# Kernel optimization log

Measured on AMD Instinct MI355X. Metric: run time of the kernel, lower is better.

The kernel has to match this reference:

```python
import jax, jax.numpy as jnp
import numpy as np

B, S, D, H, E, K = 4, 1024, 1024, 4096, 8, 2


def setup_inputs() -> dict:
    key = jax.random.key(0)
    ks = jax.random.split(key, 5)
    std = 0.02
    return {
        "x": jax.random.normal(ks[0], (B, S, D), dtype=jnp.float32),
        "router_W": jax.random.normal(ks[1], (D, E), dtype=jnp.float32) * std,
        "W_in": jax.random.normal(ks[2], (E, D, H), dtype=jnp.float32) * std,
        "b_in": jnp.zeros((E, H), dtype=jnp.float32),
        "W_out": jax.random.normal(ks[3], (E, H, D), dtype=jnp.float32) * std,
        "b_out": jnp.zeros((E, D), dtype=jnp.float32),
    }


def reference(x, router_W, W_in, b_in, W_out, b_out):
    # ---- routing ----
    logits = jnp.einsum("bsd,de->bse", x, router_W)          # [B,S,E]
    probs = jax.nn.softmax(logits, axis=-1)                    # [B,S,E]
    top_p, top_i = jax.lax.top_k(probs, K)                     # [B,S,K]
    top_p = top_p / (jnp.sum(top_p, axis=-1, keepdims=True) + 1e-8)
    one_hot = jax.nn.one_hot(top_i, E, dtype=x.dtype)          # [B,S,K,E]
    combine = jnp.sum(one_hot * top_p[..., None], axis=-2)     # [B,S,E] per-expert weight

    # ---- experts (original runs full batch through every selected expert;
    #      with E=8, K=2 all experts are active, so run all densely) ----
    h = jnp.einsum("bsd,edh->ebsh", x, W_in) + b_in[:, None, None, :]
    h = jax.nn.gelu(h, approximate=False)
    y = jnp.einsum("ebsh,ehd->ebsd", h, W_out) + b_out[:, None, None, :]
    out = jnp.einsum("bse,ebsd->bsd", combine, y)              # weighted combine

    # ---- load-balancing aux loss ----
    expert_usage = jnp.mean(one_hot, axis=(0, 1, 2))           # f_i, fraction of routed slots
    avg_probs = jnp.mean(probs, axis=(0, 1))                   # P_i
    aux_loss = E * jnp.sum(avg_probs * expert_usage)
    return out, aux_loss
```

## Files before the change

kernel.cpp:

```cpp
#include <hip/hip_runtime.h>
#include <hip/hip_bf16.h>
#include <math.h>

#define B_ 4
#define S_ 1024
#define T_ (B_ * S_)
#define D_ 1024
#define H_ 4096
#define E_ 8
#define K_ 2
#define A_ (T_ * K_)
#define MAXT_ 72

typedef __bf16 bf16x8_t __attribute__((ext_vector_type(8)));
typedef float f32x4_t __attribute__((ext_vector_type(4)));

__device__ inline unsigned short f2bf(float f) {
    __hip_bfloat16 h = __float2bfloat16(f);
    return *reinterpret_cast<unsigned short*>(&h);
}

__device__ __forceinline__ void gl2lds16(const unsigned short* g, unsigned short* l) {
    auto* gp = reinterpret_cast<const __attribute__((address_space(1))) unsigned int*>(
        reinterpret_cast<uintptr_t>(g));
    auto* lp = reinterpret_cast<__attribute__((address_space(3))) unsigned int*>(
        reinterpret_cast<uintptr_t>(l));
    __builtin_amdgcn_global_load_lds(gp, lp, 16, 0, 0);
}


__global__ void router_kernel(const float* __restrict__ x, const float* __restrict__ rw,
                              int* __restrict__ tok_e, float* __restrict__ tok_w,
                              int* __restrict__ counts_pad, float* __restrict__ probs_pad) {
    __shared__ float s_probs[E_];
    __shared__ int s_counts[E_];
    const int tid = threadIdx.x;
    if (tid < E_) { s_probs[tid] = 0.f; s_counts[tid] = 0; }
    __syncthreads();
    const int wave = tid >> 6;
    const int lane = tid & 63;

    float wprob[E_];
    int wcount[E_];
#pragma unroll
    for (int e = 0; e < E_; ++e) { wprob[e] = 0.f; wcount[e] = 0; }

    for (int tt = 0; tt < 4; ++tt) {
        const int token = blockIdx.x * 16 + wave * 4 + tt;
        const float* xr = x + (long)token * D_;
        float acc[E_];
#pragma unroll
        for (int e = 0; e < E_; ++e) acc[e] = 0.f;
        for (int i = 0; i < D_ / 64; ++i) {
            int d = i * 64 + lane;
            float xv = xr[d];
            const float* w = rw + (long)d * E_;
#pragma unroll
            for (int e = 0; e < E_; ++e) acc[e] += xv * w[e];
        }
#pragma unroll
        for (int e = 0; e < E_; ++e) {
            for (int off = 32; off > 0; off >>= 1)
                acc[e] += __shfl_down(acc[e], off);
        }
        if (lane == 0) {
            float m = acc[0];
            for (int e = 1; e < E_; ++e) m = fmaxf(m, acc[e]);
            float p[E_], s = 0.f;
            for (int e = 0; e < E_; ++e) { p[e] = expf(acc[e] - m); s += p[e]; }
            float inv = 1.f / s;
            for (int e = 0; e < E_; ++e) { p[e] *= inv; wprob[e] += p[e]; }
            int i0 = 0;
            for (int e = 1; e < E_; ++e) if (p[e] > p[i0]) i0 = e;
            int i1 = (i0 == 0) ? 1 : 0;
            for (int e = 0; e < E_; ++e) if (e != i0 && p[e] > p[i1]) i1 = e;
            float w0 = p[i0], w1 = p[i1];
            float inv2 = 1.f / (w0 + w1 + 1e-8f);
            tok_e[token * 2] = i0;
            tok_e[token * 2 + 1] = i1;
            tok_w[token * 2] = w0 * inv2;
            tok_w[token * 2 + 1] = w1 * inv2;
            wcount[i0]++; wcount[i1]++;
        }
    }
    if (lane == 0) {
#pragma unroll
        for (int e = 0; e < E_; ++e) {
            atomicAdd(&s_probs[e], wprob[e]);
            if (wcount[e]) atomicAdd(&s_counts[e], wcount[e]);
        }
    }
    __syncthreads();
    if (tid < E_) {
        atomicAdd(&probs_pad[tid * 32], s_probs[tid]);
        if (s_counts[tid]) atomicAdd(&counts_pad[tid * 32], s_counts[tid]);
    }
}

__global__ void offsets_aux_kernel(const int* __restrict__ counts_pad,
                                   const float* __restrict__ probs_pad,
                                   int* __restrict__ offsets,
                                   int* __restrict__ tile_e, int* __restrict__ tile_m,
                                   int* __restrict__ n_tiles, float* __restrict__ aux_out) {
    if (threadIdx.x == 0 && blockIdx.x == 0) {
        int run = 0, t = 0;
        for (int e = 0; e < E_; ++e) {
            int c = counts_pad[e * 32];
            offsets[e] = run;
            for (int m0 = 0; m0 < c; m0 += 128) {
                tile_e[t] = e; tile_m[t] = m0; ++t;
            }
            run += c;
        }
        offsets[E_] = run;
        *n_tiles = t;
        float aux = 0.f;
        for (int e = 0; e < E_; ++e)
            aux += (probs_pad[e * 32] / (float)T_) * ((float)counts_pad[e * 32] / (float)A_);
        *aux_out = (float)E_ * aux;
    }
}

__global__ void scatter_kernel(const int* __restrict__ tok_e, const float* __restrict__ tok_w,
                               const int* __restrict__ offsets, int* __restrict__ cursors_pad,
                               int* __restrict__ perm_token, float* __restrict__ perm_weight,
                               int* __restrict__ inv_pos) {
    int i = blockIdx.x * blockDim.x + threadIdx.x;
    int lane = threadIdx.x & 63;
    int e = tok_e[i];
    float w = tok_w[i];
    unsigned long long bal[E_];
#pragma unroll
    for (int q = 0; q < E_; ++q) bal[q] = __ballot(e == q);
    unsigned long long below = (1ull << lane) - 1ull;
    int rank = __popcll(bal[e] & below);
    int base = 0;
    if (lane < E_) {
        int c = __popcll(bal[lane]);
        if (c) base = atomicAdd(&cursors_pad[lane * 32], c);
    }
    int mybase = __shfl(base, e);
    int pos = offsets[e] + mybase + rank;
    perm_token[pos] = i >> 1;
    perm_weight[pos] = w;
    inv_pos[i] = pos;
}

__global__ void cast_x_kernel(const float* __restrict__ x, unsigned short* __restrict__ xb) {
    long i = (long)blockIdx.x * blockDim.x + threadIdx.x;
    float4 v = reinterpret_cast<const float4*>(x)[i];
    unsigned long long packed = (unsigned long long)f2bf(v.x)
        | ((unsigned long long)f2bf(v.y) << 16)
        | ((unsigned long long)f2bf(v.z) << 32)
        | ((unsigned long long)f2bf(v.w) << 48);
    reinterpret_cast<unsigned long long*>(xb)[i] = packed;
}

__global__ void transpose_cast_kernel(const float* __restrict__ in, unsigned short* __restrict__ out,
                                      int R, int C) {
    __shared__ float tile[32][33];
    long e = blockIdx.z;
    const float* in_e = in + e * (long)R * C;
    unsigned short* out_e = out + e * (long)R * C;
    int x0 = blockIdx.x * 32;
    int y0 = blockIdx.y * 32;
    int tx = threadIdx.x, ty = threadIdx.y;
#pragma unroll
    for (int i = 0; i < 4; ++i)
        tile[ty + i * 8][tx] = in_e[(long)(y0 + ty + i * 8) * C + x0 + tx];
    __syncthreads();
#pragma unroll
    for (int i = 0; i < 4; ++i)
        out_e[(long)(x0 + ty + i * 8) * R + y0 + tx] = f2bf(tile[tx][ty + i * 8]);
}

template <int PHASE>
__launch_bounds__(256, 4)
__global__ void moe_gemm_kernel(const unsigned short* __restrict__ A_src,
                                const unsigned short* __restrict__ B_src,
                                const float* __restrict__ bias,
                                const int* __restrict__ offsets,
                                const int* __restrict__ tile_e, const int* __restrict__ tile_m,
                                const int* __restrict__ p_ntiles,
                                const int* __restrict__ perm_token,
                                const float* __restrict__ perm_weight,
                                unsigned short* __restrict__ h_buf,
                                float* __restrict__ y_perm) {
    constexpr int Ksz = (PHASE == 1) ? D_ : H_;
    constexpr int Nsz = (PHASE == 1) ? H_ : D_;
    constexpr int NTX = (Nsz / 128) / 8;
    const int id = blockIdx.x;
    const int c = id & 7;
    const int r = id >> 3;
    const int mt = r % MAXT_;
    if (mt >= *p_ntiles) return;
    const int nt = c * NTX + r / MAXT_;
    const int e = tile_e[mt];
    const int m0 = tile_m[mt];
    const int off_e = offsets[e];
    const int n_e = offsets[e + 1] - off_e;
    const int n0 = nt * 128;

    __shared__ __attribute__((aligned(16))) unsigned short lds_a[2 * 128 * 32];
    __shared__ __attribute__((aligned(16))) unsigned short lds_b[2 * 128 * 32];

    const int tid = threadIdx.x;
    const int lane = tid & 63;
    const int wave = tid >> 6;
    const int wm = (wave >> 1) * 64;
    const int wn = (wave & 1) * 64;
    const int lrow = lane & 15;
    const int kg = lane >> 4;

    const unsigned short* gA[2];
    const unsigned short* gB[2];
    unsigned short* ldsA[2];
    unsigned short* ldsB[2];
#pragma unroll
    for (int j = 0; j < 2; ++j) {
        const int g = j * 4 + wave;
        const int rr = g * 16 + (lane >> 2);
        const int ch = lane & 3;
        const int sc = ch ^ ((rr >> 1) & 3);
        int m_loc = m0 + rr;
        int m_cl = (m_loc < n_e) ? m_loc : (n_e - 1);
        int pos = off_e + m_cl;
        long arow;
        if (PHASE == 1) arow = (long)perm_token[pos] * Ksz;
        else            arow = (long)pos * Ksz;
        gA[j] = A_src + arow + sc * 8;
        gB[j] = B_src + (long)e * Nsz * Ksz + (long)(n0 + rr) * Ksz + sc * 8;
        ldsA[j] = lds_a + g * 512;
        ldsB[j] = lds_b + g * 512;
    }

    int a_off[4], b_off[4];
#pragma unroll
    for (int i = 0; i < 4; ++i) {
        const int rr = wm + i * 16 + lrow;
        a_off[i] = rr * 32 + ((kg ^ ((rr >> 1) & 3)) * 8);
        const int cc = wn + i * 16 + lrow;
        b_off[i] = cc * 32 + ((kg ^ ((cc >> 1) & 3)) * 8);
    }

    f32x4_t acc[4][4];
#pragma unroll
    for (int i = 0; i < 4; ++i)
#pragma unroll
        for (int j = 0; j < 4; ++j)
            acc[i][j] = (f32x4_t){0.f, 0.f, 0.f, 0.f};

    gl2lds16(gA[0], ldsA[0]);
    gl2lds16(gA[1], ldsA[1]);
    gl2lds16(gB[0], ldsB[0]);
    gl2lds16(gB[1], ldsB[1]);

    for (int k0 = 0; k0 < Ksz; k0 += 32) {
        const int cur = (k0 >> 5) & 1;
        __syncthreads();
        if (k0 + 32 < Ksz) {
            const int nxt = cur ^ 1;
            gl2lds16(gA[0] + k0 + 32, ldsA[0] + nxt * 4096);
            gl2lds16(gA[1] + k0 + 32, ldsA[1] + nxt * 4096);
            gl2lds16(gB[0] + k0 + 32, ldsB[0] + nxt * 4096);
            gl2lds16(gB[1] + k0 + 32, ldsB[1] + nxt * 4096);
        }
        const unsigned short* la = lds_a + cur * 4096;
        const unsigned short* lb = lds_b + cur * 4096;
        bf16x8_t a_frag[4], b_frag[4];
#pragma unroll
        for (int i = 0; i < 4; ++i) {
            a_frag[i] = *reinterpret_cast<const bf16x8_t*>(&la[a_off[i]]);
            b_frag[i] = *reinterpret_cast<const bf16x8_t*>(&lb[b_off[i]]);
        }
#pragma unroll
        for (int i = 0; i < 4; ++i)
#pragma unroll
            for (int j = 0; j < 4; ++j)
                acc[i][j] = __builtin_amdgcn_mfma_f32_16x16x32_bf16(a_frag[i], b_frag[j], acc[i][j], 0, 0, 0);
    }

    const float* bias_e = bias + (long)e * Nsz;
#pragma unroll
    for (int i = 0; i < 4; ++i) {
#pragma unroll
        for (int rq = 0; rq < 4; ++rq) {
            int row_loc = wm + i * 16 + kg * 4 + rq;
            int m_loc = m0 + row_loc;
            if (m_loc >= n_e) continue;
            int pos = off_e + m_loc;
            if (PHASE == 1) {
#pragma unroll
                for (int j = 0; j < 4; ++j) {
                    int n = n0 + wn + j * 16 + lrow;
                    float v = acc[i][j][rq] + bias_e[n];
                    v = 0.5f * v * (1.0f + erff(v * 0.70710678118654752440f));
                    h_buf[(long)pos * Nsz + n] = f2bf(v);
                }
            } else {
                float wgt = perm_weight[pos];
#pragma unroll
                for (int j = 0; j < 4; ++j) {
                    int n = n0 + wn + j * 16 + lrow;
                    y_perm[(long)pos * Nsz + n] = (acc[i][j][rq] + bias_e[n]) * wgt;
                }
            }
        }
    }
}

__global__ void combine_kernel(const float* __restrict__ y_perm, const int* __restrict__ inv_pos,
                               float* __restrict__ out) {
    int t = blockIdx.x;
    int d4 = threadIdx.x;
    int p0 = inv_pos[t * 2];
    int p1 = inv_pos[t * 2 + 1];
    float4 a = reinterpret_cast<const float4*>(y_perm + (long)p0 * D_)[d4];
    float4 b = reinterpret_cast<const float4*>(y_perm + (long)p1 * D_)[d4];
    float4 o = {a.x + b.x, a.y + b.y, a.z + b.z, a.w + b.w};
    reinterpret_cast<float4*>(out + (long)t * D_)[d4] = o;
}

extern "C" void kernel_launch(void* const* d_in, const int* in_sizes, int n_in,
                              void* d_out, int out_size, void* d_ws, size_t ws_size,
                              hipStream_t stream) {
    const float* x        = (const float*)d_in[0];
    const float* router_W = (const float*)d_in[1];
    const float* W_in     = (const float*)d_in[2];
    const float* b_in     = (const float*)d_in[3];
    const float* W_out    = (const float*)d_in[4];
    const float* b_out    = (const float*)d_in[5];
    float* out = (float*)d_out;

    char* ws = (char*)d_ws;
    size_t off = 0;
    auto alloc = [&](size_t bytes) -> void* {
        void* p = ws + off;
        off += (bytes + 255) & ~(size_t)255;
        return p;
    };

    char* ctrl = (char*)alloc(4096);
    int* counts_pad   = (int*)ctrl;
    float* probs_pad  = (float*)(ctrl + 1024);
    int* cursors_pad  = (int*)(ctrl + 2048);
    int* offsets      = (int*)(ctrl + 3072);
    int* tile_e       = (int*)(ctrl + 3200);
    int* tile_m       = (int*)(ctrl + 3584);
    int* n_tiles      = (int*)(ctrl + 3968);
    int* tok_e         = (int*)alloc((size_t)A_ * 4);
    float* tok_w       = (float*)alloc((size_t)A_ * 4);
    int* perm_token    = (int*)alloc((size_t)A_ * 4);
    float* perm_weight = (float*)alloc((size_t)A_ * 4);
    int* inv_pos       = (int*)alloc((size_t)A_ * 4);
    unsigned short* x_bf    = (unsigned short*)alloc((size_t)T_ * D_ * 2);
    unsigned short* w_in_t  = (unsigned short*)alloc((size_t)E_ * D_ * H_ * 2);
    unsigned short* w_out_t = (unsigned short*)alloc((size_t)E_ * D_ * H_ * 2);
    unsigned short* h_buf   = (unsigned short*)alloc((size_t)A_ * H_ * 2);
    float* y_perm           = (float*)alloc((size_t)A_ * D_ * 4);

    hipMemsetAsync(ctrl, 0, 4096, stream);

    cast_x_kernel<<<(T_ * D_ / 4) / 256, 256, 0, stream>>>(x, x_bf);
    transpose_cast_kernel<<<dim3(H_ / 32, D_ / 32, E_), dim3(32, 8), 0, stream>>>(W_in, w_in_t, D_, H_);
    transpose_cast_kernel<<<dim3(D_ / 32, H_ / 32, E_), dim3(32, 8), 0, stream>>>(W_out, w_out_t, H_, D_);
    router_kernel<<<T_ / 16, 256, 0, stream>>>(x, router_W, tok_e, tok_w, counts_pad, probs_pad);
    offsets_aux_kernel<<<1, 64, 0, stream>>>(counts_pad, probs_pad, offsets,
                                             tile_e, tile_m, n_tiles, out + (out_size - 1));
    scatter_kernel<<<A_ / 256, 256, 0, stream>>>(tok_e, tok_w, offsets, cursors_pad,
                                                 perm_token, perm_weight, inv_pos);

    moe_gemm_kernel<1><<<8 * MAXT_ * (H_ / 128 / 8), 256, 0, stream>>>(
        x_bf, w_in_t, b_in, offsets, tile_e, tile_m, n_tiles,
        perm_token, perm_weight, h_buf, y_perm);
    moe_gemm_kernel<2><<<8 * MAXT_ * (D_ / 128 / 8), 256, 0, stream>>>(
        h_buf, w_out_t, b_out, offsets, tile_e, tile_m, n_tiles,
        perm_token, perm_weight, h_buf, y_perm);
    combine_kernel<<<T_, 256, 0, stream>>>(y_perm, inv_pos, out);
}
```

Measured before the change: 661.1 us.

## Enlarge MoE GEMM tiles, triple-buffer K pipeline, add split-K and XCD remap

The grouped GEMM now uses 256x128 tiles with 512 threads, a K step of 64, and a three-stage global_load_lds pipeline with explicit barriers, setprio and waitcnt. Blocks are remapped so consecutive work lands on the same XCD. The second GEMM can split K in two into separate partial buffers when the workspace is large enough, and the combine kernel sums those partials. The weight transpose-cast kernel is rewritten with 64x64 tiles and vectorized loads and stores. The aim is better data reuse and MFMA utilisation, at the cost of more LDS, lower occupancy, padding waste on partial 256-row tiles, and extra partial-sum traffic when split-K is on.

Result: slower. 682.7 us (+3.3%).

```diff
diff --git a/kernel.cpp b/kernel.cpp
--- a/kernel.cpp
+++ b/kernel.cpp
@@ -10,10 +10,11 @@
 #define E_ 8
 #define K_ 2
 #define A_ (T_ * K_)
-#define MAXT_ 72
+#define NTM_ 40
 
 typedef __bf16 bf16x8_t __attribute__((ext_vector_type(8)));
 typedef float f32x4_t __attribute__((ext_vector_type(4)));
+typedef unsigned short u16x8_t __attribute__((ext_vector_type(8)));
 
 __device__ inline unsigned short f2bf(float f) {
     __hip_bfloat16 h = __float2bfloat16(f);
@@ -107,7 +108,7 @@
         for (int e = 0; e < E_; ++e) {
             int c = counts_pad[e * 32];
             offsets[e] = run;
-            for (int m0 = 0; m0 < c; m0 += 128) {
+            for (int m0 = 0; m0 < c; m0 += 256) {
                 tile_e[t] = e; tile_m[t] = m0; ++t;
             }
             run += c;
@@ -158,24 +159,36 @@
 
 __global__ void transpose_cast_kernel(const float* __restrict__ in, unsigned short* __restrict__ out,
                                       int R, int C) {
-    __shared__ float tile[32][33];
-    long e = blockIdx.z;
+    __shared__ float tile[64][65];
+    const long e = blockIdx.z;
     const float* in_e = in + e * (long)R * C;
     unsigned short* out_e = out + e * (long)R * C;
-    int x0 = blockIdx.x * 32;
-    int y0 = blockIdx.y * 32;
-    int tx = threadIdx.x, ty = threadIdx.y;
-#pragma unroll
-    for (int i = 0; i < 4; ++i)
-        tile[ty + i * 8][tx] = in_e[(long)(y0 + ty + i * 8) * C + x0 + tx];
+    const int c0 = blockIdx.x * 64;
+    const int r0 = blockIdx.y * 64;
+    const int tid = threadIdx.x;
+    const int c4 = (tid & 15) * 4;
+    const int rb = tid >> 4;
+#pragma unroll
+    for (int i = 0; i < 4; ++i) {
+        const int r = rb + i * 16;
+        const float4 v = *reinterpret_cast<const float4*>(&in_e[(long)(r0 + r) * C + c0 + c4]);
+        tile[r][c4] = v.x; tile[r][c4 + 1] = v.y; tile[r][c4 + 2] = v.z; tile[r][c4 + 3] = v.w;
+    }
     __syncthreads();
-#pragma unroll
-    for (int i = 0; i < 4; ++i)
-        out_e[(long)(x0 + ty + i * 8) * R + y0 + tx] = f2bf(tile[tx][ty + i * 8]);
-}
-
-template <int PHASE>
-__launch_bounds__(256, 4)
+    const int rs = (tid & 7) * 8;
+    const int cb = tid >> 3;
+#pragma unroll
+    for (int i = 0; i < 2; ++i) {
+        const int c = cb + i * 32;
+        u16x8_t p;
+#pragma unroll
+        for (int j = 0; j < 8; ++j) p[j] = f2bf(tile[rs + j][c]);
+        *reinterpret_cast<u16x8_t*>(&out_e[(long)(c0 + c) * R + r0 + rs]) = p;
+    }
+}
+
+template <int PHASE, int NSPLIT>
+__launch_bounds__(512, 2)
 __global__ void moe_gemm_kernel(const unsigned short* __restrict__ A_src,
                                 const unsigned short* __restrict__ B_src,
                                 const float* __restrict__ bias,
@@ -186,123 +199,186 @@
                                 const float* __restrict__ perm_weight,
                                 unsigned short* __restrict__ h_buf,
                                 float* __restrict__ y_perm) {
-    constexpr int Ksz = (PHASE == 1) ? D_ : H_;
-    constexpr int Nsz = (PHASE == 1) ? H_ : D_;
-    constexpr int NTX = (Nsz / 128) / 8;
+    constexpr int Ksz  = (PHASE == 1) ? D_ : H_;
+    constexpr int Kloc = (PHASE == 1) ? D_ : (H_ / NSPLIT);
+    constexpr int Nsz  = (PHASE == 1) ? H_ : D_;
+    constexpr int NT   = Kloc / 64;
+    constexpr int NTN  = Nsz / 128;
+
+    const int nwg = gridDim.x;
     const int id = blockIdx.x;
-    const int c = id & 7;
-    const int r = id >> 3;
-    const int mt = r % MAXT_;
+    const int q = nwg >> 3, r8 = nwg & 7;
+    const int xcd = id & 7, sub = id >> 3;
+    const int wg = (xcd < r8 ? xcd * (q + 1) : r8 * (q + 1) + (xcd - r8) * q) + sub;
+    const int mt = wg % NTM_;
     if (mt >= *p_ntiles) return;
-    const int nt = c * NTX + r / MAXT_;
+    const int rest = wg / NTM_;
+    const int nt = rest % NTN;
+    const int kh = rest / NTN;
     const int e = tile_e[mt];
     const int m0 = tile_m[mt];
     const int off_e = offsets[e];
     const int n_e = offsets[e + 1] - off_e;
     const int n0 = nt * 128;
-
-    __shared__ __attribute__((aligned(16))) unsigned short lds_a[2 * 128 * 32];
-    __shared__ __attribute__((aligned(16))) unsigned short lds_b[2 * 128 * 32];
+    const long k_base = (long)kh * Kloc;
+
+    __shared__ __attribute__((aligned(16))) unsigned short lds_a[3 * 256 * 64];
+    __shared__ __attribute__((aligned(16))) unsigned short lds_b[3 * 128 * 64];
 
     const int tid = threadIdx.x;
     const int lane = tid & 63;
     const int wave = tid >> 6;
-    const int wm = (wave >> 1) * 64;
-    const int wn = (wave & 1) * 64;
+    const int wr = wave >> 1;
+    const int wc = wave & 1;
     const int lrow = lane & 15;
     const int kg = lane >> 4;
 
-    const unsigned short* gA[2];
+    const unsigned short* gA[4];
     const unsigned short* gB[2];
-    unsigned short* ldsA[2];
-    unsigned short* ldsB[2];
-#pragma unroll
-    for (int j = 0; j < 2; ++j) {
-        const int g = j * 4 + wave;
-        const int rr = g * 16 + (lane >> 2);
-        const int ch = lane & 3;
-        const int sc = ch ^ ((rr >> 1) & 3);
-        int m_loc = m0 + rr;
-        int m_cl = (m_loc < n_e) ? m_loc : (n_e - 1);
-        int pos = off_e + m_cl;
+    int dstA[4], dstB[2];
+#pragma unroll
+    for (int j = 0; j < 4; ++j) {
+        const int chunk = j * 512 + tid;
+        const int rr = chunk >> 3;
+        const int ch = tid & 7;
+        const int m_loc = m0 + rr;
+        const int m_cl = (m_loc < n_e) ? m_loc : (n_e - 1);
+        const int pos = off_e + m_cl;
         long arow;
         if (PHASE == 1) arow = (long)perm_token[pos] * Ksz;
         else            arow = (long)pos * Ksz;
-        gA[j] = A_src + arow + sc * 8;
-        gB[j] = B_src + (long)e * Nsz * Ksz + (long)(n0 + rr) * Ksz + sc * 8;
-        ldsA[j] = lds_a + g * 512;
-        ldsB[j] = lds_b + g * 512;
-    }
-
-    int a_off[4], b_off[4];
-#pragma unroll
-    for (int i = 0; i < 4; ++i) {
-        const int rr = wm + i * 16 + lrow;
-        a_off[i] = rr * 32 + ((kg ^ ((rr >> 1) & 3)) * 8);
-        const int cc = wn + i * 16 + lrow;
-        b_off[i] = cc * 32 + ((kg ^ ((cc >> 1) & 3)) * 8);
-    }
+        gA[j] = A_src + arow + k_base + ((ch ^ (rr & 7)) * 8);
+        dstA[j] = (j * 512 + wave * 64) * 8;
+    }
+#pragma unroll
+    for (int j = 0; j < 2; ++j) {
+        const int chunk = j * 512 + tid;
+        const int rr = chunk >> 3;
+        const int ch = tid & 7;
+        gB[j] = B_src + (long)e * Nsz * Ksz + (long)(n0 + rr) * Ksz + k_base + ((ch ^ (rr & 7)) * 8);
+        dstB[j] = (j * 512 + wave * 64) * 8;
+    }
+
+    int aoff[2][4], boff[2][4];
+#pragma unroll
+    for (int kf = 0; kf < 2; ++kf)
+#pragma unroll
+        for (int i = 0; i < 4; ++i) {
+            const int r = wr * 64 + i * 16 + lrow;
+            aoff[kf][i] = r * 64 + (((kf * 4 + kg) ^ (r & 7)) * 8);
+            const int c = wc * 64 + i * 16 + lrow;
+            boff[kf][i] = c * 64 + (((kf * 4 + kg) ^ (c & 7)) * 8);
+        }
 
     f32x4_t acc[4][4];
 #pragma unroll
     for (int i = 0; i < 4; ++i)
 #pragma unroll
-        for (int j = 0; j < 4; ++j)
-            acc[i][j] = (f32x4_t){0.f, 0.f, 0.f, 0.f};
-
-    gl2lds16(gA[0], ldsA[0]);
-    gl2lds16(gA[1], ldsA[1]);
-    gl2lds16(gB[0], ldsB[0]);
-    gl2lds16(gB[1], ldsB[1]);
-
-    for (int k0 = 0; k0 < Ksz; k0 += 32) {
-        const int cur = (k0 >> 5) & 1;
-        __syncthreads();
-        if (k0 + 32 < Ksz) {
-            const int nxt = cur ^ 1;
-            gl2lds16(gA[0] + k0 + 32, ldsA[0] + nxt * 4096);
-            gl2lds16(gA[1] + k0 + 32, ldsA[1] + nxt * 4096);
-            gl2lds16(gB[0] + k0 + 32, ldsB[0] + nxt * 4096);
-            gl2lds16(gB[1] + k0 + 32, ldsB[1] + nxt * 4096);
-        }
-        const unsigned short* la = lds_a + cur * 4096;
-        const unsigned short* lb = lds_b + cur * 4096;
-        bf16x8_t a_frag[4], b_frag[4];
+        for (int j = 0; j < 4; ++j) acc[i][j] = (f32x4_t){0.f, 0.f, 0.f, 0.f};
+
+#pragma unroll
+    for (int tt = 0; tt < 2; ++tt) {
+        gl2lds16(gA[0] + tt * 64, lds_a + tt * 16384 + dstA[0]);
+        gl2lds16(gA[1] + tt * 64, lds_a + tt * 16384 + dstA[1]);
+        gl2lds16(gB[0] + tt * 64, lds_b + tt * 8192 + dstB[0]);
+        gl2lds16(gA[2] + tt * 64, lds_a + tt * 16384 + dstA[2]);
+        gl2lds16(gA[3] + tt * 64, lds_a + tt * 16384 + dstA[3]);
+        gl2lds16(gB[1] + tt * 64, lds_b + tt * 8192 + dstB[1]);
+    }
+    asm volatile("s_waitcnt vmcnt(6)" ::: "memory");
+    __builtin_amdgcn_s_barrier();
+
+    for (int t = 0; t < NT; ++t) {
+        const int s = t % 3;
+        const int s2 = (t + 2) % 3;
+        const unsigned short* la = lds_a + s * 16384;
+        const unsigned short* lb = lds_b + s * 8192;
+        const bool pf = (t + 2 < NT);
+
+        bf16x8_t a0[4], b0[4];
+#pragma unroll
+        for (int i = 0; i < 4; ++i) a0[i] = *reinterpret_cast<const bf16x8_t*>(la + aoff[0][i]);
+#pragma unroll
+        for (int i = 0; i < 4; ++i) b0[i] = *reinterpret_cast<const bf16x8_t*>(lb + boff[0][i]);
+        if (pf) {
+            gl2lds16(gA[0] + (t + 2) * 64, lds_a + s2 * 16384 + dstA[0]);
+            gl2lds16(gA[1] + (t + 2) * 64, lds_a + s2 * 16384 + dstA[1]);
+            gl2lds16(gB[0] + (t + 2) * 64, lds_b + s2 * 8192 + dstB[0]);
+        }
+        __builtin_amdgcn_s_barrier();
+        asm volatile("s_waitcnt lgkmcnt(0)" ::: "memory");
+        __builtin_amdgcn_sched_barrier(0);
+        __builtin_amdgcn_s_setprio(1);
+#pragma unroll
+        for (int i = 0; i < 4; ++i)
+#pragma unroll
+            for (int j = 0; j < 4; ++j)
+                acc[i][j] = __builtin_amdgcn_mfma_f32_16x16x32_bf16(a0[i], b0[j], acc[i][j], 0, 0, 0);
+        __builtin_amdgcn_s_setprio(0);
+        __builtin_amdgcn_s_barrier();
+
+        bf16x8_t a1[4], b1[4];
+#pragma unroll
+        for (int i = 0; i < 4; ++i) a1[i] = *reinterpret_cast<const bf16x8_t*>(la + aoff[1][i]);
+#pragma unroll
+        for (int i = 0; i < 4; ++i) b1[i] = *reinterpret_cast<const bf16x8_t*>(lb + boff[1][i]);
+        if (pf) {
+            gl2lds16(gA[2] + (t + 2) * 64, lds_a + s2 * 16384 + dstA[2]);
+            gl2lds16(gA[3] + (t + 2) * 64, lds_a + s2 * 16384 + dstA[3]);
+            gl2lds16(gB[1] + (t + 2) * 64, lds_b + s2 * 8192 + dstB[1]);
+        }
+        __builtin_amdgcn_s_barrier();
+        asm volatile("s_waitcnt lgkmcnt(0)" ::: "memory");
+        __builtin_amdgcn_sched_barrier(0);
+        __builtin_amdgcn_s_setprio(1);
+#pragma unroll
+        for (int i = 0; i < 4; ++i)
+#pragma unroll
+            for (int j = 0; j < 4; ++j)
+                acc[i][j] = __builtin_amdgcn_mfma_f32_16x16x32_bf16(a1[i], b1[j], acc[i][j], 0, 0, 0);
+        __builtin_amdgcn_s_setprio(0);
+        if (t + 1 < NT) {
+            if (t + 2 < NT) asm volatile("s_waitcnt vmcnt(6)" ::: "memory");
+            else            asm volatile("s_waitcnt vmcnt(0)" ::: "memory");
+        }
+        __builtin_amdgcn_s_barrier();
+    }
+
+    const float* bias_e = bias + (long)e * Nsz;
+    if (PHASE == 1) {
 #pragma unroll
         for (int i = 0; i < 4; ++i) {
-            a_frag[i] = *reinterpret_cast<const bf16x8_t*>(&la[a_off[i]]);
-            b_frag[i] = *reinterpret_cast<const bf16x8_t*>(&lb[b_off[i]]);
-        }
-#pragma unroll
-        for (int i = 0; i < 4; ++i)
-#pragma unroll
-            for (int j = 0; j < 4; ++j)
-                acc[i][j] = __builtin_amdgcn_mfma_f32_16x16x32_bf16(a_frag[i], b_frag[j], acc[i][j], 0, 0, 0);
-    }
-
-    const float* bias_e = bias + (long)e * Nsz;
-#pragma unroll
-    for (int i = 0; i < 4; ++i) {
-#pragma unroll
-        for (int rq = 0; rq < 4; ++rq) {
-            int row_loc = wm + i * 16 + kg * 4 + rq;
-            int m_loc = m0 + row_loc;
-            if (m_loc >= n_e) continue;
-            int pos = off_e + m_loc;
-            if (PHASE == 1) {
+#pragma unroll
+            for (int rq = 0; rq < 4; ++rq) {
+                const int row_loc = wr * 64 + i * 16 + kg * 4 + rq;
+                const int m_loc = m0 + row_loc;
+                if (m_loc >= n_e) continue;
+                const int pos = off_e + m_loc;
 #pragma unroll
                 for (int j = 0; j < 4; ++j) {
-                    int n = n0 + wn + j * 16 + lrow;
+                    const int n = n0 + wc * 64 + j * 16 + lrow;
                     float v = acc[i][j][rq] + bias_e[n];
                     v = 0.5f * v * (1.0f + erff(v * 0.70710678118654752440f));
                     h_buf[(long)pos * Nsz + n] = f2bf(v);
                 }
-            } else {
-                float wgt = perm_weight[pos];
+            }
+        }
+    } else {
+        float* yp = y_perm + (long)kh * ((long)A_ * D_);
+#pragma unroll
+        for (int i = 0; i < 4; ++i) {
+#pragma unroll
+            for (int rq = 0; rq < 4; ++rq) {
+                const int row_loc = wr * 64 + i * 16 + kg * 4 + rq;
+                const int m_loc = m0 + row_loc;
+                if (m_loc >= n_e) continue;
+                const int pos = off_e + m_loc;
+                const float wgt = perm_weight[pos];
 #pragma unroll
                 for (int j = 0; j < 4; ++j) {
-                    int n = n0 + wn + j * 16 + lrow;
-                    y_perm[(long)pos * Nsz + n] = (acc[i][j][rq] + bias_e[n]) * wgt;
+                    const int n = n0 + wc * 64 + j * 16 + lrow;
+                    float v = acc[i][j][rq] + ((kh == 0) ? bias_e[n] : 0.f);
+                    yp[(long)pos * Nsz + n] = v * wgt;
                 }
             }
         }
@@ -310,14 +386,21 @@
 }
 
 __global__ void combine_kernel(const float* __restrict__ y_perm, const int* __restrict__ inv_pos,
-                               float* __restrict__ out) {
+                               float* __restrict__ out, int splitk) {
     int t = blockIdx.x;
     int d4 = threadIdx.x;
     int p0 = inv_pos[t * 2];
     int p1 = inv_pos[t * 2 + 1];
-    float4 a = reinterpret_cast<const float4*>(y_perm + (long)p0 * D_)[d4];
-    float4 b = reinterpret_cast<const float4*>(y_perm + (long)p1 * D_)[d4];
+    const float4* y0 = reinterpret_cast<const float4*>(y_perm);
+    float4 a = y0[(long)p0 * (D_ / 4) + d4];
+    float4 b = y0[(long)p1 * (D_ / 4) + d4];
     float4 o = {a.x + b.x, a.y + b.y, a.z + b.z, a.w + b.w};
+    if (splitk) {
+        const float4* y1 = reinterpret_cast<const float4*>(y_perm + (long)A_ * D_);
+        float4 c = y1[(long)p0 * (D_ / 4) + d4];
+        float4 d = y1[(long)p1 * (D_ / 4) + d4];
+        o.x += c.x + d.x; o.y += c.y + d.y; o.z += c.z + d.z; o.w += c.w + d.w;
+    }
     reinterpret_cast<float4*>(out + (long)t * D_)[d4] = o;
 }
 
@@ -339,6 +422,8 @@
         off += (bytes + 255) & ~(size_t)255;
         return p;
     };
+
+    const int splitk = (ws_size >= (size_t)290 * 1024 * 1024) ? 1 : 0;
 
     char* ctrl = (char*)alloc(4096);
     int* counts_pad   = (int*)ctrl;
@@ -357,24 +442,30 @@
     unsigned short* w_in_t  = (unsigned short*)alloc((size_t)E_ * D_ * H_ * 2);
     unsigned short* w_out_t = (unsigned short*)alloc((size_t)E_ * D_ * H_ * 2);
     unsigned short* h_buf   = (unsigned short*)alloc((size_t)A_ * H_ * 2);
-    float* y_perm           = (float*)alloc((size_t)A_ * D_ * 4);
+    float* y_perm           = (float*)alloc((size_t)(1 + splitk) * A_ * D_ * 4);
 
     hipMemsetAsync(ctrl, 0, 4096, stream);
 
     cast_x_kernel<<<(T_ * D_ / 4) / 256, 256, 0, stream>>>(x, x_bf);
-    transpose_cast_kernel<<<dim3(H_ / 32, D_ / 32, E_), dim3(32, 8), 0, stream>>>(W_in, w_in_t, D_, H_);
-    transpose_cast_kernel<<<dim3(D_ / 32, H_ / 32, E_), dim3(32, 8), 0, stream>>>(W_out, w_out_t, H_, D_);
+    transpose_cast_kernel<<<dim3(H_ / 64, D_ / 64, E_), 256, 0, stream>>>(W_in, w_in_t, D_, H_);
+    transpose_cast_kernel<<<dim3(D_ / 64, H_ / 64, E_), 256, 0, stream>>>(W_out, w_out_t, H_, D_);
     router_kernel<<<T_ / 16, 256, 0, stream>>>(x, router_W, tok_e, tok_w, counts_pad, probs_pad);
     offsets_aux_kernel<<<1, 64, 0, stream>>>(counts_pad, probs_pad, offsets,
                                              tile_e, tile_m, n_tiles, out + (out_size - 1));
     scatter_kernel<<<A_ / 256, 256, 0, stream>>>(tok_e, tok_w, offsets, cursors_pad,
                                                  perm_token, perm_weight, inv_pos);
 
-    moe_gemm_kernel<1><<<8 * MAXT_ * (H_ / 128 / 8), 256, 0, stream>>>(
+    moe_gemm_kernel<1, 1><<<NTM_ * (H_ / 128), 512, 0, stream>>>(
         x_bf, w_in_t, b_in, offsets, tile_e, tile_m, n_tiles,
         perm_token, perm_weight, h_buf, y_perm);
-    moe_gemm_kernel<2><<<8 * MAXT_ * (D_ / 128 / 8), 256, 0, stream>>>(
-        h_buf, w_out_t, b_out, offsets, tile_e, tile_m, n_tiles,
-        perm_token, perm_weight, h_buf, y_perm);
-    combine_kernel<<<T_, 256, 0, stream>>>(y_perm, inv_pos, out);
-}
+    if (splitk) {
+        moe_gemm_kernel<2, 2><<<NTM_ * (D_ / 128) * 2, 512, 0, stream>>>(
+            h_buf, w_out_t, b_out, offsets, tile_e, tile_m, n_tiles,
+            perm_token, perm_weight, h_buf, y_perm);
+    } else {
+        moe_gemm_kernel<2, 1><<<NTM_ * (D_ / 128), 512, 0, stream>>>(
+            h_buf, w_out_t, b_out, offsets, tile_e, tile_m, n_tiles,
+            perm_token, perm_weight, h_buf, y_perm);
+    }
+    combine_kernel<<<T_, 256, 0, stream>>>(y_perm, inv_pos, out, splitk);
+}
```
